# Optimization experiments

Hardware: AMD Instinct MI355X
Metric: run time of the kernel (lower is better)

Reference implementation:

```python
import jax, jax.numpy as jnp
import numpy as np

NUM_VARS = 22
LAYERS = 2
N = 2 ** NUM_VARS


def setup_inputs() -> dict:
    key = jax.random.key(0)
    k1, k2, k3, k4 = jax.random.split(key, 4)
    h = jax.random.normal(k1, (N,), dtype=jnp.float32)          # unsatisfied-clause 'energy' per bitstring
    hS = jax.random.uniform(k2, (N,), dtype=jnp.float32)        # satisfiability weight per bitstring
    gamma = jax.random.normal(k3, (LAYERS,), dtype=jnp.float32) * 0.01
    beta = jax.random.normal(k4, (LAYERS,), dtype=jnp.float32) * 0.01
    return {"h": h, "hS": hS, "gamma": gamma, "beta": beta}


def reference(h, hS, gamma, beta):
    n = NUM_VARS
    # |+>^n initial state: uniform amplitudes 1/sqrt(N)
    circuit = jnp.full((N,), 1.0 / np.sqrt(N), dtype=jnp.complex64)
    for l in range(LAYERS):
        # cost unitary: elementwise phase exp(i * gamma * h)
        circuit = jnp.exp((1j * gamma[l] * h).astype(jnp.complex64)) * circuit
        # mixing unitary: per-qubit X-rotation butterfly.
        # torch's transpose(0,i)+split+cat swaps the two slices along qubit axis i,
        # which for a size-2 axis is exactly a flip along that axis.
        cb = jnp.cos(beta[l]).astype(jnp.complex64)
        sb = (1j * jnp.sin(beta[l])).astype(jnp.complex64)
        c = circuit.reshape((2,) * n)
        for i in range(n):  # fixed small loop over qubits (structurally distinct axes)
            c = cb * c + sb * jnp.flip(c, axis=i)
        circuit = c.reshape(N)
    ps = jnp.real(circuit * jnp.conj(circuit))  # |amplitude|^2
    return jnp.dot(ps, hS)
```

## Files before the change

kernel.cpp:

```cpp
#include <hip/hip_runtime.h>


#define NTOT    (1u << 22)
#define LO_BITS 14
#define HI_BITS 8
#define LO      (1u << LO_BITS)
#define HI      (1u << HI_BITS)
#define GRP     64
#define TPB     1024
#define R       16

typedef __fp16 h2_t __attribute__((ext_vector_type(2)));
union PkU { unsigned u; h2_t h; };

__device__ __forceinline__ unsigned pk(float x, float y) {
    PkU p; p.h = __builtin_amdgcn_cvt_pkrtz(x, y); return p.u;
}
__device__ __forceinline__ float2 unpk(unsigned v) {
    PkU p; p.u = v; return make_float2((float)p.h.x, (float)p.h.y);
}

#define REGSTAGE(MASK, CB, SB) {                                  \
    _Pragma("unroll")                                             \
    for (int r0 = 0; r0 < R; ++r0) {                              \
        if ((r0 & (MASK)) == 0) {                                 \
            const int r1 = r0 | (MASK);                           \
            float t0r = re[r0], t0i = im[r0];                     \
            float t1r = re[r1], t1i = im[r1];                     \
            re[r0] = (CB) * t0r - (SB) * t1i;                     \
            im[r0] = (CB) * t0i + (SB) * t1r;                     \
            re[r1] = (CB) * t1r - (SB) * t0i;                     \
            im[r1] = (CB) * t1i + (SB) * t0r;                     \
        } } }

#define SHFLSTAGE(MASK, CB, SB) {                                 \
    _Pragma("unroll")                                             \
    for (int r = 0; r < R; ++r) {                                 \
        unsigned pv = (unsigned)__shfl_xor((int)pk(re[r], im[r]), (MASK), 64); \
        float2 p = unpk(pv);                                      \
        float tr = re[r], ti = im[r];                             \
        re[r] = (CB) * tr - (SB) * p.y;                           \
        im[r] = (CB) * ti + (SB) * p.x;                           \
    } }

__global__ __launch_bounds__(TPB, 4) void k_init_low(
    const float* __restrict__ h, const float* __restrict__ gam,
    const float* __restrict__ bet, unsigned* __restrict__ st,
    float* __restrict__ out)
{
    __shared__ unsigned sC[LO];
    const float g1 = gam[0];
    const float cb = __cosf(bet[0]), sb = __sinf(bet[0]);
    const unsigned t = threadIdx.x, lane = t & 63u, w = t >> 6;
    const size_t base = (size_t)blockIdx.x * LO;
    float re[R], im[R];

    if (blockIdx.x == 0 && t == 0) out[0] = 0.f;

    #pragma unroll
    for (int r = 0; r < R; ++r) {
        float s, c;
        __sincosf(g1 * h[base + ((unsigned)r << 10) + t], &s, &c);
        re[r] = c * 0x1p-11f;
        im[r] = s * 0x1p-11f;
    }
    REGSTAGE(1, cb, sb)  REGSTAGE(2, cb, sb)
    REGSTAGE(4, cb, sb)  REGSTAGE(8, cb, sb)
    SHFLSTAGE(1,  cb, sb) SHFLSTAGE(2,  cb, sb)
    SHFLSTAGE(4,  cb, sb) SHFLSTAGE(8,  cb, sb)
    SHFLSTAGE(16, cb, sb) SHFLSTAGE(32, cb, sb)
    #pragma unroll
    for (int r = 0; r < R; ++r) sC[((unsigned)r << 10) | t] = pk(re[r], im[r]);
    __syncthreads();
    #pragma unroll
    for (int r = 0; r < R; ++r) {
        unsigned j = (w << 10) | ((unsigned)r << 6) | lane;
        float2 v = unpk(sC[j]); re[r] = v.x; im[r] = v.y;
    }
    REGSTAGE(1, cb, sb)  REGSTAGE(2, cb, sb)
    REGSTAGE(4, cb, sb)  REGSTAGE(8, cb, sb)
    #pragma unroll
    for (int r = 0; r < R; ++r) {
        unsigned j = (w << 10) | ((unsigned)r << 6) | lane;
        st[base + j] = pk(re[r], im[r]);
    }
}

__global__ __launch_bounds__(TPB, 4) void k_high(
    const float* __restrict__ h, const float* __restrict__ gam,
    const float* __restrict__ bet, unsigned* __restrict__ st)
{
    __shared__ unsigned sC[GRP * HI];
    const float g2  = gam[1];
    const float cb1 = __cosf(bet[0]), sb1 = __sinf(bet[0]);
    const float cb2 = __cosf(bet[1]), sb2 = __sinf(bet[1]);
    const unsigned t = threadIdx.x, g = t & 63u, w = t >> 6;
    const unsigned lo0 = blockIdx.x * GRP;
    float re[R], im[R], hv[R];

    #pragma unroll
    for (int r = 0; r < R; ++r) {
        unsigned hi = w | ((unsigned)r << 4);
        float2 v = unpk(st[(size_t)hi * LO + lo0 + g]);
        re[r] = v.x; im[r] = v.y;
    }
    #pragma unroll
    for (int r = 0; r < R; ++r) {
        unsigned hi = (unsigned)r | (w << 4);
        hv[r] = h[(size_t)hi * LO + lo0 + g];
    }
    REGSTAGE(1, cb1, sb1)  REGSTAGE(2, cb1, sb1)
    REGSTAGE(4, cb1, sb1)  REGSTAGE(8, cb1, sb1)
    #pragma unroll
    for (int r = 0; r < R; ++r)
        sC[g | (w << 6) | ((unsigned)r << 10)] = pk(re[r], im[r]);
    __syncthreads();
    #pragma unroll
    for (int r = 0; r < R; ++r) {
        float2 v = unpk(sC[g | ((unsigned)r << 6) | (w << 10)]);
        re[r] = v.x; im[r] = v.y;
    }
    REGSTAGE(1, cb1, sb1)  REGSTAGE(2, cb1, sb1)
    REGSTAGE(4, cb1, sb1)  REGSTAGE(8, cb1, sb1)
    #pragma unroll
    for (int r = 0; r < R; ++r) {
        float s, c;
        __sincosf(g2 * hv[r], &s, &c);
        float tr = re[r], ti = im[r];
        re[r] = tr * c - ti * s;
        im[r] = tr * s + ti * c;
    }
    REGSTAGE(1, cb2, sb2)  REGSTAGE(2, cb2, sb2)
    REGSTAGE(4, cb2, sb2)  REGSTAGE(8, cb2, sb2)
    __syncthreads();
    #pragma unroll
    for (int r = 0; r < R; ++r)
        sC[g | ((unsigned)r << 6) | (w << 10)] = pk(re[r], im[r]);
    __syncthreads();
    #pragma unroll
    for (int r = 0; r < R; ++r) {
        float2 v = unpk(sC[g | (w << 6) | ((unsigned)r << 10)]);
        re[r] = v.x; im[r] = v.y;
    }
    REGSTAGE(1, cb2, sb2)  REGSTAGE(2, cb2, sb2)
    REGSTAGE(4, cb2, sb2)  REGSTAGE(8, cb2, sb2)
    #pragma unroll
    for (int r = 0; r < R; ++r) {
        unsigned hi = w | ((unsigned)r << 4);
        st[(size_t)hi * LO + lo0 + g] = pk(re[r], im[r]);
    }
}

__global__ __launch_bounds__(TPB, 4) void k_low2(
    const float* __restrict__ hS, const float* __restrict__ bet,
    const unsigned* __restrict__ st, float* __restrict__ out)
{
    __shared__ unsigned sC[LO];
    const float cb = __cosf(bet[1]), sb = __sinf(bet[1]);
    const unsigned t = threadIdx.x, lane = t & 63u, w = t >> 6;
    const size_t base = (size_t)blockIdx.x * LO;
    float re[R], im[R], hv[R];

    #pragma unroll
    for (int r = 0; r < R; ++r) {
        float2 v = unpk(st[base + ((unsigned)r << 10) + t]);
        re[r] = v.x; im[r] = v.y;
    }
    #pragma unroll
    for (int r = 0; r < R; ++r) {
        unsigned j = (w << 10) | ((unsigned)r << 6) | lane;
        hv[r] = hS[base + j];
    }
    REGSTAGE(1, cb, sb)  REGSTAGE(2, cb, sb)
    REGSTAGE(4, cb, sb)  REGSTAGE(8, cb, sb)
    SHFLSTAGE(1,  cb, sb) SHFLSTAGE(2,  cb, sb)
    SHFLSTAGE(4,  cb, sb) SHFLSTAGE(8,  cb, sb)
    SHFLSTAGE(16, cb, sb) SHFLSTAGE(32, cb, sb)
    #pragma unroll
    for (int r = 0; r < R; ++r) sC[((unsigned)r << 10) | t] = pk(re[r], im[r]);
    __syncthreads();
    #pragma unroll
    for (int r = 0; r < R; ++r) {
        unsigned j = (w << 10) | ((unsigned)r << 6) | lane;
        float2 v = unpk(sC[j]); re[r] = v.x; im[r] = v.y;
    }
    REGSTAGE(1, cb, sb)  REGSTAGE(2, cb, sb)
    REGSTAGE(4, cb, sb)  REGSTAGE(8, cb, sb)
    float acc = 0.f;
    #pragma unroll
    for (int r = 0; r < R; ++r)
        acc = fmaf(re[r] * re[r] + im[r] * im[r], hv[r], acc);
    #pragma unroll
    for (int off = 32; off >= 1; off >>= 1)
        acc += __shfl_down(acc, off, 64);
    __syncthreads();
    if (lane == 0) ((float*)sC)[w] = acc;
    __syncthreads();
    if (t == 0) {
        float s = 0.f;
        #pragma unroll
        for (int ww = 0; ww < TPB / 64; ++ww) s += ((float*)sC)[ww];
        unsafeAtomicAdd(out, s);
    }
}

extern "C" void kernel_launch(void* const* d_in, const int* in_sizes, int n_in,
                              void* d_out, int out_size, void* d_ws, size_t ws_size,
                              hipStream_t stream)
{
    (void)in_sizes; (void)n_in; (void)out_size; (void)ws_size;
    const float* h   = (const float*)d_in[0];
    const float* hS  = (const float*)d_in[1];
    const float* gam = (const float*)d_in[2];
    const float* bet = (const float*)d_in[3];
    unsigned* st = (unsigned*)d_ws;
    float* out   = (float*)d_out;

    k_init_low<<<dim3(NTOT / LO), dim3(TPB), 0, stream>>>(h, gam, bet, st, out);
    k_high    <<<dim3(LO / GRP),  dim3(TPB), 0, stream>>>(h, gam, bet, st);
    k_low2    <<<dim3(NTOT / LO), dim3(TPB), 0, stream>>>(hS, bet, st, out);
}
```

Before: 119.4 us.

## Fuse three phases into one cooperative kernel with grid syncs and vectorized loads

Merges the three kernel launches into a single cooperative kernel of 256 blocks that separates the phases with grid-wide syncs, and falls back to three launches if the cooperative launch fails. The aim is to remove the launch gaps between kernels. It also changes the low-qubit index mapping so that h and the state are read and written as float4/uint4 and shared memory is stored with 16-byte accesses, which cuts the number of memory instructions. In exchange it pays for grid.sync and a cooperative launch, and keeps only 256 blocks resident with no overlap between phases.

```diff
diff --git a/kernel.cpp b/kernel.cpp
--- a/kernel.cpp
+++ b/kernel.cpp
@@ -1,11 +1,13 @@
 #include <hip/hip_runtime.h>
+#include <hip/hip_cooperative_groups.h>
+
+namespace cg = cooperative_groups;
 
 
 #define NTOT    (1u << 22)
 #define LO_BITS 14
-#define HI_BITS 8
 #define LO      (1u << LO_BITS)
-#define HI      (1u << HI_BITS)
+#define HI      256u
 #define GRP     64
 #define TPB     1024
 #define R       16
@@ -43,26 +45,31 @@
         im[r] = (CB) * ti + (SB) * p.x;                           \
     } }
 
-__global__ __launch_bounds__(TPB, 4) void k_init_low(
-    const float* __restrict__ h, const float* __restrict__ gam,
+__device__ __forceinline__ void phase1(
+    unsigned* sC, const float* __restrict__ h, const float* __restrict__ gam,
     const float* __restrict__ bet, unsigned* __restrict__ st,
-    float* __restrict__ out)
-{
-    __shared__ unsigned sC[LO];
+    float* __restrict__ out, unsigned b)
+{
     const float g1 = gam[0];
     const float cb = __cosf(bet[0]), sb = __sinf(bet[0]);
     const unsigned t = threadIdx.x, lane = t & 63u, w = t >> 6;
-    const size_t base = (size_t)blockIdx.x * LO;
+    const size_t base = (size_t)b * LO;
     float re[R], im[R];
 
-    if (blockIdx.x == 0 && t == 0) out[0] = 0.f;
-
-    #pragma unroll
-    for (int r = 0; r < R; ++r) {
-        float s, c;
-        __sincosf(g1 * h[base + ((unsigned)r << 10) + t], &s, &c);
-        re[r] = c * 0x1p-11f;
-        im[r] = s * 0x1p-11f;
+    if (b == 0 && t == 0) out[0] = 0.f;
+
+    #pragma unroll
+    for (int rh = 0; rh < 4; ++rh) {
+        float4 h4 = *(const float4*)(h + base +
+                        (((unsigned)rh << 12) | (w << 8) | (lane << 2)));
+        const float hv4[4] = {h4.x, h4.y, h4.z, h4.w};
+        #pragma unroll
+        for (int rl = 0; rl < 4; ++rl) {
+            float s, c;
+            __sincosf(g1 * hv4[rl], &s, &c);
+            re[rh * 4 + rl] = c * 0x1p-11f;
+            im[rh * 4 + rl] = s * 0x1p-11f;
+        }
     }
     REGSTAGE(1, cb, sb)  REGSTAGE(2, cb, sb)
     REGSTAGE(4, cb, sb)  REGSTAGE(8, cb, sb)
@@ -70,32 +77,35 @@
     SHFLSTAGE(4,  cb, sb) SHFLSTAGE(8,  cb, sb)
     SHFLSTAGE(16, cb, sb) SHFLSTAGE(32, cb, sb)
     #pragma unroll
-    for (int r = 0; r < R; ++r) sC[((unsigned)r << 10) | t] = pk(re[r], im[r]);
-    __syncthreads();
-    #pragma unroll
-    for (int r = 0; r < R; ++r) {
-        unsigned j = (w << 10) | ((unsigned)r << 6) | lane;
-        float2 v = unpk(sC[j]); re[r] = v.x; im[r] = v.y;
-    }
-    REGSTAGE(1, cb, sb)  REGSTAGE(2, cb, sb)
-    REGSTAGE(4, cb, sb)  REGSTAGE(8, cb, sb)
-    #pragma unroll
-    for (int r = 0; r < R; ++r) {
-        unsigned j = (w << 10) | ((unsigned)r << 6) | lane;
-        st[base + j] = pk(re[r], im[r]);
-    }
-}
-
-__global__ __launch_bounds__(TPB, 4) void k_high(
-    const float* __restrict__ h, const float* __restrict__ gam,
-    const float* __restrict__ bet, unsigned* __restrict__ st)
-{
-    __shared__ unsigned sC[GRP * HI];
+    for (int rh = 0; rh < 4; ++rh) {
+        unsigned u4[4];
+        #pragma unroll
+        for (int rl = 0; rl < 4; ++rl) u4[rl] = pk(re[rh * 4 + rl], im[rh * 4 + rl]);
+        *(uint4*)&sC[((unsigned)rh << 12) | (w << 8) | (lane << 2)] = *(const uint4*)u4;
+    }
+    __syncthreads();
+    #pragma unroll
+    for (int q = 0; q < R; ++q) {
+        float2 v = unpk(sC[((w >> 2) << 12) | ((unsigned)q << 8) | ((w & 3u) << 6) | lane]);
+        re[q] = v.x; im[q] = v.y;
+    }
+    REGSTAGE(1, cb, sb)  REGSTAGE(2, cb, sb)
+    REGSTAGE(4, cb, sb)  REGSTAGE(8, cb, sb)
+    #pragma unroll
+    for (int q = 0; q < R; ++q)
+        st[base + (((w >> 2) << 12) | ((unsigned)q << 8) | ((w & 3u) << 6) | lane)]
+            = pk(re[q], im[q]);
+}
+
+__device__ __forceinline__ void phase2(
+    unsigned* sC, const float* __restrict__ h, const float* __restrict__ gam,
+    const float* __restrict__ bet, unsigned* __restrict__ st, unsigned b)
+{
     const float g2  = gam[1];
     const float cb1 = __cosf(bet[0]), sb1 = __sinf(bet[0]);
     const float cb2 = __cosf(bet[1]), sb2 = __sinf(bet[1]);
     const unsigned t = threadIdx.x, g = t & 63u, w = t >> 6;
-    const unsigned lo0 = blockIdx.x * GRP;
+    const unsigned lo0 = b * GRP;
     float re[R], im[R], hv[R];
 
     #pragma unroll
@@ -151,45 +161,54 @@
     }
 }
 
-__global__ __launch_bounds__(TPB, 4) void k_low2(
-    const float* __restrict__ hS, const float* __restrict__ bet,
-    const unsigned* __restrict__ st, float* __restrict__ out)
-{
-    __shared__ unsigned sC[LO];
+__device__ __forceinline__ void phase3(
+    unsigned* sC, const float* __restrict__ hS, const float* __restrict__ bet,
+    const unsigned* __restrict__ st, float* __restrict__ out, unsigned b)
+{
     const float cb = __cosf(bet[1]), sb = __sinf(bet[1]);
     const unsigned t = threadIdx.x, lane = t & 63u, w = t >> 6;
-    const size_t base = (size_t)blockIdx.x * LO;
+    const size_t base = (size_t)b * LO;
     float re[R], im[R], hv[R];
 
     #pragma unroll
-    for (int r = 0; r < R; ++r) {
-        float2 v = unpk(st[base + ((unsigned)r << 10) + t]);
-        re[r] = v.x; im[r] = v.y;
-    }
-    #pragma unroll
-    for (int r = 0; r < R; ++r) {
-        unsigned j = (w << 10) | ((unsigned)r << 6) | lane;
-        hv[r] = hS[base + j];
-    }
+    for (int rh = 0; rh < 4; ++rh) {
+        uint4 u4 = *(const uint4*)&st[base +
+                        (((unsigned)rh << 12) | (w << 8) | (lane << 2))];
+        const unsigned uu[4] = {u4.x, u4.y, u4.z, u4.w};
+        #pragma unroll
+        for (int rl = 0; rl < 4; ++rl) {
+            float2 v = unpk(uu[rl]);
+            re[rh * 4 + rl] = v.x; im[rh * 4 + rl] = v.y;
+        }
+    }
+    #pragma unroll
+    for (int q = 0; q < R; ++q)
+        hv[q] = hS[base + (((w >> 2) << 12) | ((unsigned)q << 8) | ((w & 3u) << 6) | lane)];
+
     REGSTAGE(1, cb, sb)  REGSTAGE(2, cb, sb)
     REGSTAGE(4, cb, sb)  REGSTAGE(8, cb, sb)
     SHFLSTAGE(1,  cb, sb) SHFLSTAGE(2,  cb, sb)
     SHFLSTAGE(4,  cb, sb) SHFLSTAGE(8,  cb, sb)
     SHFLSTAGE(16, cb, sb) SHFLSTAGE(32, cb, sb)
     #pragma unroll
-    for (int r = 0; r < R; ++r) sC[((unsigned)r << 10) | t] = pk(re[r], im[r]);
-    __syncthreads();
-    #pragma unroll
-    for (int r = 0; r < R; ++r) {
-        unsigned j = (w << 10) | ((unsigned)r << 6) | lane;
-        float2 v = unpk(sC[j]); re[r] = v.x; im[r] = v.y;
+    for (int rh = 0; rh < 4; ++rh) {
+        unsigned u4[4];
+        #pragma unroll
+        for (int rl = 0; rl < 4; ++rl) u4[rl] = pk(re[rh * 4 + rl], im[rh * 4 + rl]);
+        *(uint4*)&sC[((unsigned)rh << 12) | (w << 8) | (lane << 2)] = *(const uint4*)u4;
+    }
+    __syncthreads();
+    #pragma unroll
+    for (int q = 0; q < R; ++q) {
+        float2 v = unpk(sC[((w >> 2) << 12) | ((unsigned)q << 8) | ((w & 3u) << 6) | lane]);
+        re[q] = v.x; im[q] = v.y;
     }
     REGSTAGE(1, cb, sb)  REGSTAGE(2, cb, sb)
     REGSTAGE(4, cb, sb)  REGSTAGE(8, cb, sb)
     float acc = 0.f;
     #pragma unroll
-    for (int r = 0; r < R; ++r)
-        acc = fmaf(re[r] * re[r] + im[r] * im[r], hv[r], acc);
+    for (int q = 0; q < R; ++q)
+        acc = fmaf(re[q] * re[q] + im[q] * im[q], hv[q], acc);
     #pragma unroll
     for (int off = 32; off >= 1; off >>= 1)
         acc += __shfl_down(acc, off, 64);
@@ -199,9 +218,47 @@
     if (t == 0) {
         float s = 0.f;
         #pragma unroll
-        for (int ww = 0; ww < TPB / 64; ++ww) s += ((float*)sC)[ww];
+        for (int ww = 0; ww < (int)(TPB / 64); ++ww) s += ((float*)sC)[ww];
         unsafeAtomicAdd(out, s);
     }
+}
+
+__global__ __launch_bounds__(TPB, 4) void k_fused(
+    const float* __restrict__ h, const float* __restrict__ hS,
+    const float* __restrict__ gam, const float* __restrict__ bet,
+    unsigned* __restrict__ st, float* __restrict__ out)
+{
+    __shared__ unsigned sC[LO];
+    cg::grid_group grid = cg::this_grid();
+    const unsigned b = blockIdx.x;
+    phase1(sC, h, gam, bet, st, out, b);
+    grid.sync();
+    phase2(sC, h, gam, bet, st, b);
+    grid.sync();
+    phase3(sC, hS, bet, st, out, b);
+}
+
+__global__ __launch_bounds__(TPB, 4) void k_p1(
+    const float* __restrict__ h, const float* __restrict__ gam,
+    const float* __restrict__ bet, unsigned* __restrict__ st,
+    float* __restrict__ out)
+{
+    __shared__ unsigned sC[LO];
+    phase1(sC, h, gam, bet, st, out, blockIdx.x);
+}
+__global__ __launch_bounds__(TPB, 4) void k_p2(
+    const float* __restrict__ h, const float* __restrict__ gam,
+    const float* __restrict__ bet, unsigned* __restrict__ st)
+{
+    __shared__ unsigned sC[LO];
+    phase2(sC, h, gam, bet, st, blockIdx.x);
+}
+__global__ __launch_bounds__(TPB, 4) void k_p3(
+    const float* __restrict__ hS, const float* __restrict__ bet,
+    const unsigned* __restrict__ st, float* __restrict__ out)
+{
+    __shared__ unsigned sC[LO];
+    phase3(sC, hS, bet, st, out, blockIdx.x);
 }
 
 extern "C" void kernel_launch(void* const* d_in, const int* in_sizes, int n_in,
@@ -216,7 +273,13 @@
     unsigned* st = (unsigned*)d_ws;
     float* out   = (float*)d_out;
 
-    k_init_low<<<dim3(NTOT / LO), dim3(TPB), 0, stream>>>(h, gam, bet, st, out);
-    k_high    <<<dim3(LO / GRP),  dim3(TPB), 0, stream>>>(h, gam, bet, st);
-    k_low2    <<<dim3(NTOT / LO), dim3(TPB), 0, stream>>>(hS, bet, st, out);
-}
+    void* ka[] = {(void*)&h, (void*)&hS, (void*)&gam, (void*)&bet,
+                  (void*)&st, (void*)&out};
+    hipError_t e = hipLaunchCooperativeKernel((const void*)k_fused,
+                        dim3(NTOT / LO), dim3(TPB), ka, 0, stream);
+    if (e != hipSuccess) {
+        k_p1<<<dim3(NTOT / LO), dim3(TPB), 0, stream>>>(h, gam, bet, st, out);
+        k_p2<<<dim3(LO / GRP),  dim3(TPB), 0, stream>>>(h, gam, bet, st);
+        k_p3<<<dim3(NTOT / LO), dim3(TPB), 0, stream>>>(hS, bet, st, out);
+    }
+}
```

Result: slower. 212.2 us (+77.8%).
